# Kernel optimization log

Measured on AMD Instinct MI355X. Metric: run time of the kernel, lower is better.

## Reference

```python
import jax, jax.numpy as jnp
import numpy as np
from jax import lax

NC = 80
REG_MAX = 16
BINS = REG_MAX + 1
RADIUS = 2.5
TOPK = 10
L_BOX, L_CLS, L_DFL = 7.5, 1.0, 1.5


def focal_bce(x, t, alpha=0.25, gamma=2.0):
    # numerically stable BCE-with-logits: max(x,0) - x*t + log1p(exp(-|x|))
    p = jax.nn.sigmoid(x)
    ce = jnp.maximum(x, 0.0) - x * t + jnp.log1p(jnp.exp(-jnp.abs(x)))
    p_t = p * t + (1.0 - p) * (1.0 - t)
    a_t = alpha * t + (1.0 - alpha) * (1.0 - t)
    return ce * a_t * (1.0 - p_t) ** gamma


def _level_loss(reg, cls, boxes, labels, stride):
    B, _, H, W = reg.shape
    HW = H * W
    G = boxes.shape[1]
    gy, gx = jnp.meshgrid(jnp.arange(H, dtype=jnp.float32), jnp.arange(W, dtype=jnp.float32), indexing='ij')
    centers = jnp.stack([gx + 0.5, gy + 0.5], -1).reshape(HW, 2)  # [HW,2]
    gt = boxes / stride  # [B,G,4]
    gctr = (gt[..., :2] + gt[..., 2:]) * 0.5  # [B,G,2]
    cx = centers[None, :, None, 0]
    cy = centers[None, :, None, 1]
    dl = cx - gt[:, None, :, 0]
    dt = cy - gt[:, None, :, 1]
    dr = gt[:, None, :, 2] - cx
    db = gt[:, None, :, 3] - cy
    in_gt = (dl > 0) & (dt > 0) & (dr > 0) & (db > 0)
    in_ctr = ((cx >= gctr[:, None, :, 0] - RADIUS) & (cx <= gctr[:, None, :, 0] + RADIUS)
              & (cy >= gctr[:, None, :, 1] - RADIUS) & (cy <= gctr[:, None, :, 1] + RADIUS))
    mask = in_gt & in_ctr  # [B,HW,G]
    any_pos = jnp.any(mask, axis=(1, 2))  # [B]
    # fallback: topk closest anchor centers per GT (smallest distance along point dim)
    dist = jnp.sqrt(((centers[None, :, None, :] - gctr[:, None, :, :]) ** 2).sum(-1))  # [B,HW,G]
    k = min(TOPK, HW)
    _, idx = lax.top_k(-jnp.swapaxes(dist, 1, 2), k)  # [B,G,k]
    fb = jnp.zeros((B, HW, G), bool).at[jnp.arange(B)[:, None, None], idx, jnp.arange(G)[None, :, None]].set(True)
    mask = jnp.where(any_pos[:, None, None], mask, fb)
    mf = mask.astype(jnp.float32)
    n_pos = mf.sum((1, 2))  # [B] (>=1 by construction of fallback)

    cls_flat = cls.transpose(0, 2, 3, 1).reshape(B, HW, NC)
    reg_flat = reg.transpose(0, 2, 3, 1).reshape(B, HW, 4, BINS)

    # ---- DFL ----
    ltrb = jnp.clip(jnp.stack([dl, dt, dr, db], -1), 0.0)  # [B,HW,G,4]
    tgt = jnp.clip(ltrb, 0.0, REG_MAX - 1e-4)
    lb = jnp.floor(tgt).astype(jnp.int32)
    rb = jnp.minimum(lb + 1, REG_MAX)
    wl = rb.astype(jnp.float32) - tgt
    wr = tgt - lb.astype(jnp.float32)
    logp = jax.nn.log_softmax(reg_flat, -1)  # [B,HW,4,BINS]
    bi = jnp.arange(B)[:, None, None, None]
    pi = jnp.arange(HW)[None, :, None, None]
    ki = jnp.arange(4)[None, None, None, :]
    dfl_pair = -(logp[bi, pi, ki, lb] * wl + logp[bi, pi, ki, rb] * wr)  # [B,HW,G,4]
    dfl = ((dfl_pair * mf[..., None]).sum((1, 2, 3)) / (n_pos * 4.0)).sum()

    # ---- box (IoU, detached as in original) ----
    prob = jax.nn.softmax(reg_flat, -1)
    d = (prob * jnp.arange(BINS, dtype=jnp.float32)).sum(-1)  # [B,HW,4]
    pcx = centers[None, :, 0]
    pcy = centers[None, :, 1]
    pred_box = jnp.stack([pcx - d[..., 0], pcy - d[..., 1], pcx + d[..., 2], pcy + d[..., 3]], -1)  # [B,HW,4]
    b1 = pred_box[:, :, None, :]
    b2 = gt[:, None, :, :]
    iw = jnp.clip(jnp.minimum(b1[..., 2:], b2[..., 2:]) - jnp.maximum(b1[..., :2], b2[..., :2]), 0.0)
    inter = iw[..., 0] * iw[..., 1]
    a1 = (b1[..., 2] - b1[..., 0]) * (b1[..., 3] - b1[..., 1])
    a2 = (b2[..., 2] - b2[..., 0]) * (b2[..., 3] - b2[..., 1])
    iou = lax.stop_gradient(inter / (a1 + a2 - inter + 1e-6))  # [B,HW,G]
    box = ((1.0 - iou) * mf).sum()

    # ---- cls (focal BCE, soft IoU targets). Decompose one-hot target:
    # per positive pair: sum_c f(logit_c,0) - f(logit_cls,0) + f(logit_cls,iou)
    fz = focal_bce(cls_flat, 0.0)  # [B,HW,NC]
    fz_sum = fz.sum(-1)  # [B,HW]
    bi2 = jnp.arange(B)[:, None, None]
    pi2 = jnp.arange(HW)[None, :, None]
    ci = labels[:, None, :]  # [B,1,G]
    cls_at = cls_flat[bi2, pi2, ci]  # [B,HW,G]
    fz_at = fz[bi2, pi2, ci]
    cls_pos = ((fz_sum[:, :, None] - fz_at + focal_bce(cls_at, iou)) * mf).sum()
    pos_pt = jnp.any(mask, -1)  # [B,HW]
    cls_neg = jnp.where(pos_pt, 0.0, fz_sum).sum()
    return box, cls_pos + cls_neg, dfl


def _total(reg0, cls0, reg1, cls1, reg2, cls2, gt_boxes, gt_labels):
    tb = tc = td = 0.0
    for r, c, s in ((reg0, cls0, 8.0), (reg1, cls1, 16.0), (reg2, cls2, 32.0)):
        b, cl, d = _level_loss(r, c, gt_boxes, gt_labels, s)
        tb = tb + b
        tc = tc + cl
        td = td + d
    loss = L_BOX * tb + L_CLS * tc + L_DFL * td
    return loss, tb, tc, td


def setup_inputs() -> dict:
    key = jax.random.key(0)
    ks = jax.random.split(key, 10)
    B, G = 16, 32
    d = {}
    for i, (h, w) in enumerate(((80, 80), (40, 40), (20, 20))):
        d[f'reg{i}'] = jax.random.normal(ks[2 * i], (B, 4 * BINS, h, w), jnp.float32)
        d[f'cls{i}'] = jax.random.normal(ks[2 * i + 1], (B, NC, h, w), jnp.float32)
    ctr = jax.random.uniform(ks[6], (B, G, 2), minval=0.0, maxval=640.0)
    wh = jax.random.uniform(ks[7], (B, G, 2), minval=16.0, maxval=160.0)
    x1y1 = jnp.clip(ctr - wh * 0.5, 0.0, 640.0)
    x2y2 = jnp.clip(ctr + wh * 0.5, 0.0, 640.0)
    d['gt_boxes'] = jnp.concatenate([x1y1, x2y2], -1)
    d['gt_labels'] = jax.random.randint(ks[8], (B, G), 0, NC, jnp.int32)
    return d


def reference(reg0, cls0, reg1, cls1, reg2, cls2, gt_boxes, gt_labels):
    return _total(reg0, cls0, reg1, cls1, reg2, cls2, gt_boxes, gt_labels)
```

## Files before the change

### kernel.cpp

```cpp
#include <hip/hip_runtime.h>
#include <math.h>

#define NCLS 80
#define BINS 17
#define REGMAX 16
#define NG 32
#define NB 16
#define KTOP 10
#define RAD 2.5f

#define WS_ACC   0
#define WS_NPOS  32
#define WS_DFLN  224
#define WS_ANYP  416
#define WS_CNT   608
#define WS_FB    640
#define NBLOCKS  (67 * 16)

__device__ __forceinline__ float focal0(float x) {
    float e   = __expf(-fabsf(x));
    float inv = 1.0f / (1.0f + e);
    float p   = (x >= 0.0f) ? inv : e * inv;
    float ce  = fmaxf(x, 0.0f) + __logf(1.0f + e);
    return ce * 0.75f * p * p;
}

__device__ __forceinline__ float focal_t(float x, float t) {
    float e   = __expf(-fabsf(x));
    float inv = 1.0f / (1.0f + e);
    float p   = (x >= 0.0f) ? inv : e * inv;
    float ce  = fmaxf(x, 0.0f) - x * t + __logf(1.0f + e);
    float pt  = p * t + (1.0f - p) * (1.0f - t);
    float at  = 0.25f * t + 0.75f * (1.0f - t);
    float om  = 1.0f - pt;
    return ce * at * om * om;
}

__global__ void k_prep(const float* __restrict__ gtb,
                       float* __restrict__ acc, float* __restrict__ npos,
                       float* __restrict__ dfln, int* __restrict__ anyp,
                       int* __restrict__ cnt, int* __restrict__ fb) {
    int lvl = blockIdx.x;
    int tid = threadIdx.x;
    int b = tid >> 5, g = tid & 31;
    int W = (lvl == 0) ? 80 : (lvl == 1 ? 40 : 20);
    float inv_s = (lvl == 0) ? 0.125f : (lvl == 1 ? 0.0625f : 0.03125f);
    if (lvl == 0) {
        if (tid < 2)  acc[tid] = 0.0f;
        if (tid < 48) { npos[tid] = 0.0f; dfln[tid] = 0.0f; }
        if (tid == 48) *cnt = 0;
    }
    __shared__ int s_any[NB];
    if (tid < NB) s_any[tid] = 0;
    __syncthreads();

    const float* bb = gtb + (b * NG + g) * 4;
    float x1 = bb[0] * inv_s, y1 = bb[1] * inv_s;
    float x2 = bb[2] * inv_s, y2 = bb[3] * inv_s;
    float gcx = (x1 + x2) * 0.5f, gcy = (y1 + y2) * 0.5f;
    int j0 = max((int)floorf(gcx) - 4, 0), j1 = min((int)floorf(gcx) + 4, W - 1);
    int i0 = max((int)floorf(gcy) - 4, 0), i1 = min((int)floorf(gcy) + 4, W - 1);
    bool any = false;
    for (int i = i0; i <= i1; ++i) {
        float cy = (float)i + 0.5f;
        for (int j = j0; j <= j1; ++j) {
            float cx = (float)j + 0.5f;
            bool m = (cx - x1 > 0.0f) && (cy - y1 > 0.0f) &&
                     (x2 - cx > 0.0f) && (y2 - cy > 0.0f) &&
                     (cx >= gcx - RAD) && (cx <= gcx + RAD) &&
                     (cy >= gcy - RAD) && (cy <= gcy + RAD);
            any = any || m;
        }
    }
    if (any) atomicOr(&s_any[b], 1);
    __syncthreads();
    if (g == 0) anyp[lvl * NB + b] = s_any[b];

    if (!s_any[b]) {
        float bd[KTOP]; int bi[KTOP];
        for (int t = 0; t < KTOP; ++t) { bd[t] = 3.0e38f; bi[t] = 0; }
        int HW = W * W;
        for (int p = 0; p < HW; ++p) {
            float cx = (float)(p % W) + 0.5f;
            float cy = (float)(p / W) + 0.5f;
            float dx = cx - gcx, dy = cy - gcy;
            float d = dx * dx + dy * dy;
            if (d < bd[KTOP - 1]) {
                int t = KTOP - 1;
                while (t > 0 && d < bd[t - 1]) { bd[t] = bd[t-1]; bi[t] = bi[t-1]; --t; }
                bd[t] = d; bi[t] = p;
            }
        }
        int* o = fb + ((lvl * NB + b) * NG + g) * KTOP;
        for (int t = 0; t < KTOP; ++t) o[t] = bi[t];
    }
}

__global__ __launch_bounds__(256, 4) void k_main_f(
    const float* __restrict__ reg0, const float* __restrict__ cls0,
    const float* __restrict__ reg1, const float* __restrict__ cls1,
    const float* __restrict__ reg2, const float* __restrict__ cls2,
    const float* __restrict__ gtb,  const int* __restrict__ lab,
    const int* __restrict__ anyp,   const int* __restrict__ fb,
    float* __restrict__ acc, float* __restrict__ npos, float* __restrict__ dfln,
    int* __restrict__ cnt, float* __restrict__ out)
{
    int bx = blockIdx.x;
    int b  = blockIdx.y;
    int lvl, tix, W; const float *regp, *clsp; float inv_s;
    if (bx < 50)      { lvl = 0; tix = bx;      W = 80; regp = reg0; clsp = cls0; inv_s = 0.125f;   }
    else if (bx < 63) { lvl = 1; tix = bx - 50; W = 40; regp = reg1; clsp = cls1; inv_s = 0.0625f;  }
    else              { lvl = 2; tix = bx - 63; W = 20; regp = reg2; clsp = cls2; inv_s = 0.03125f; }
    int HW = W * W;
    int tile = tix * 128;

    int lane = threadIdx.x & 63;
    int s    = threadIdx.x >> 6;
    int q0   = tile + 2 * lane;
    bool v   = q0 < HW;
    int qc   = v ? q0 : 0;
    int ri0  = qc / W, ci0 = qc - ri0 * W;
    float cx0 = (float)ci0 + 0.5f, cy0 = (float)ri0 + 0.5f;
    int ci1 = ci0 + 1, ri1 = ri0; if (ci1 == W) { ci1 = 0; ri1 = ri0 + 1; }
    float cx1 = (float)ci1 + 0.5f, cy1 = (float)ri1 + 0.5f;

    int base_r = (b * 4 * BINS) * HW + qc;
    int base_c = (b * NCLS) * HW + qc;

    __shared__ float s_dv[4][128], s_lz[4][128], s_fz[4][128];
    __shared__ unsigned char s_ps[4][128];
    __shared__ float s_bx[NG][6];
    __shared__ int   s_lab[NG];

    if (threadIdx.x < NG) {
        int g = threadIdx.x;
        float4 bb4 = *(const float4*)(gtb + (b * NG + g) * 4);
        float x1 = bb4.x * inv_s, y1 = bb4.y * inv_s;
        float x2 = bb4.z * inv_s, y2 = bb4.w * inv_s;
        s_bx[g][0] = x1; s_bx[g][1] = y1; s_bx[g][2] = x2; s_bx[g][3] = y2;
        s_bx[g][4] = (x1 + x2) * 0.5f; s_bx[g][5] = (y1 + y2) * 0.5f;
        s_lab[g] = lab[b * NG + g];
    }

    float2 rv[BINS];
#pragma unroll
    for (int t = 0; t < BINS; ++t)
        rv[t] = *(const float2*)(regp + base_r + (s * BINS + t) * HW);
    float2 cv[20];
#pragma unroll
    for (int t = 0; t < 20; ++t)
        cv[t] = *(const float2*)(clsp + base_c + (s * 20 + t) * HW);

    {
        float m0 = rv[0].x, m1 = rv[0].y;
#pragma unroll
        for (int t = 1; t < BINS; ++t) { m0 = fmaxf(m0, rv[t].x); m1 = fmaxf(m1, rv[t].y); }
        float sa = 0.f, ea = 0.f, sb = 0.f, eb = 0.f;
#pragma unroll
        for (int t = 0; t < BINS; ++t) {
            float a = __expf(rv[t].x - m0), c = __expf(rv[t].y - m1);
            sa += a; ea += a * (float)t; sb += c; eb += c * (float)t;
        }
        s_dv[s][2*lane]   = ea / sa;  s_lz[s][2*lane]   = __logf(sa) + m0;
        s_dv[s][2*lane+1] = eb / sb;  s_lz[s][2*lane+1] = __logf(sb) + m1;
    }
    {
        float fz0 = 0.f, fz1 = 0.f;
#pragma unroll
        for (int t = 0; t < 20; ++t) { fz0 += focal0(cv[t].x); fz1 += focal0(cv[t].y); }
        s_fz[s][2*lane] = fz0; s_fz[s][2*lane+1] = fz1;
    }
    __syncthreads();

    float dv0[4], lz0v[4], dv1[4], lz1v[4];
#pragma unroll
    for (int k = 0; k < 4; ++k) {
        dv0[k] = s_dv[k][2*lane];   lz0v[k] = s_lz[k][2*lane];
        dv1[k] = s_dv[k][2*lane+1]; lz1v[k] = s_lz[k][2*lane+1];
    }
    float fzs0 = s_fz[0][2*lane]   + s_fz[1][2*lane]   + s_fz[2][2*lane]   + s_fz[3][2*lane];
    float fzs1 = s_fz[0][2*lane+1] + s_fz[1][2*lane+1] + s_fz[2][2*lane+1] + s_fz[3][2*lane+1];

    float px1_0 = cx0 - dv0[0], py1_0 = cy0 - dv0[1];
    float px2_0 = cx0 + dv0[2], py2_0 = cy0 + dv0[3];
    float pa0 = (px2_0 - px1_0) * (py2_0 - py1_0);
    float px1_1 = cx1 - dv1[0], py1_1 = cy1 - dv1[1];
    float px2_1 = cx1 + dv1[2], py2_1 = cy1 + dv1[3];
    float pa1 = (px2_1 - px1_1) * (py2_1 - py1_1);

    bool anyb = anyp[lvl * NB + b] != 0;
    float bxa = 0.f, cla = 0.f, dfa = 0.f, np = 0.f;
    bool posi0 = false, posi1 = false;

#define HEAVY(G, CX, CY, DL, DT, DR, DB, PX1, PY1, PX2, PY2, PA, LZ, FZS, OFF) do { \
    float ix1 = fmaxf(PX1, x1), iy1 = fmaxf(PY1, y1);                    \
    float ix2 = fminf(PX2, x2), iy2 = fminf(PY2, y2);                    \
    float iw = fmaxf(ix2 - ix1, 0.f), ih = fmaxf(iy2 - iy1, 0.f);        \
    float inter = iw * ih;                                               \
    float ga = (x2 - x1) * (y2 - y1);                                    \
    float iou = inter / (PA + ga - inter + 1e-6f);                       \
    bxa += 1.f - iou; np += 1.f;                                         \
    float ltrb[4] = { DL, DT, DR, DB };                                  \
    _Pragma("unroll")                                                    \
    for (int k = 0; k < 4; ++k) {                                        \
        float tt = fminf(fmaxf(ltrb[k], 0.f), 15.9999f);                 \
        float lf = floorf(tt); int lb = (int)lf;                         \
        int rb = lb + 1 > REGMAX ? REGMAX : lb + 1;                      \
        float wl = (float)rb - tt, wr = tt - lf;                         \
        float xl = regp[base_r + OFF + (k * BINS + lb) * HW];            \
        float xr = regp[base_r + OFF + (k * BINS + rb) * HW];            \
        dfa -= (xl - LZ[k]) * wl + (xr - LZ[k]) * wr;                    \
    }                                                                    \
    int c = s_lab[G];                                                    \
    float xat = clsp[base_c + OFF + c * HW];                             \
    cla += FZS - focal0(xat) + focal_t(xat, iou);                        \
} while (0)

#define PROC_G(G, GEOM) do {                                             \
    float x1 = s_bx[G][0], y1 = s_bx[G][1];                              \
    float x2 = s_bx[G][2], y2 = s_bx[G][3];                              \
    float dl0 = cx0 - x1, dt0 = cy0 - y1, dr0 = x2 - cx0, db0 = y2 - cy0;\
    float dl1 = cx1 - x1, dt1 = cy1 - y1, dr1 = x2 - cx1, db1 = y2 - cy1;\
    bool m0, m1;                                                         \
    if (GEOM) {                                                          \
        float gx = s_bx[G][4], gy = s_bx[G][5];                          \
        m0 = (dl0 > 0.f) && (dt0 > 0.f) && (dr0 > 0.f) && (db0 > 0.f) && \
             (cx0 >= gx - RAD) && (cx0 <= gx + RAD) &&                   \
             (cy0 >= gy - RAD) && (cy0 <= gy + RAD);                     \
        m1 = (dl1 > 0.f) && (dt1 > 0.f) && (dr1 > 0.f) && (db1 > 0.f) && \
             (cx1 >= gx - RAD) && (cx1 <= gx + RAD) &&                   \
             (cy1 >= gy - RAD) && (cy1 <= gy + RAD);                     \
    } else {                                                             \
        const int* fbp = fb + ((lvl * NB + b) * NG + (G)) * KTOP;        \
        m0 = false; m1 = false;                                          \
        _Pragma("unroll")                                                \
        for (int t = 0; t < KTOP; ++t) {                                 \
            int f = fbp[t]; m0 = m0 || (f == q0); m1 = m1 || (f == q0+1);\
        }                                                                \
    }                                                                    \
    m0 = m0 && v; m1 = m1 && v;                                          \
    if (__any(m0 || m1)) {                                               \
        if (m0) HEAVY((G), cx0, cy0, dl0, dt0, dr0, db0,                 \
                      px1_0, py1_0, px2_0, py2_0, pa0, lz0v, fzs0, 0);   \
        if (m1) HEAVY((G), cx1, cy1, dl1, dt1, dr1, db1,                 \
                      px1_1, py1_1, px2_1, py2_1, pa1, lz1v, fzs1, 1);   \
    }                                                                    \
    posi0 = posi0 || m0; posi1 = posi1 || m1;                            \
} while (0)

    if (anyb) {
        int gg = lane & 31;
        float gy1 = s_bx[gg][1], gy2 = s_bx[gg][3], gcy = s_bx[gg][5];
        int r0 = tile / W;
        int r1 = min(tile + 127, HW - 1) / W;
        float cyLo = (float)r0 + 0.5f, cyHi = (float)r1 + 0.5f;
        bool act = (cyHi > gy1) && (gy2 > cyLo) &&
                   (cyHi >= gcy - RAD) && (cyLo <= gcy + RAD);
        unsigned long long bm = __ballot(act);
        unsigned m32 = (unsigned)(bm | (bm >> 32));
        int ord = 0;
        while (m32) {
            int g = __builtin_ctz(m32); m32 &= m32 - 1;
            if ((ord++ & 3) == s) PROC_G(g, true);
        }
    } else {
        for (int t = 0; t < 8; ++t) { int g = s * 8 + t; PROC_G(g, false); }
    }

    s_ps[s][2*lane] = posi0; s_ps[s][2*lane+1] = posi1;
    __syncthreads();
    if (s == 0) {
        int pg0 = s_ps[0][2*lane] | s_ps[1][2*lane] | s_ps[2][2*lane] | s_ps[3][2*lane];
        int pg1 = s_ps[0][2*lane+1] | s_ps[1][2*lane+1] | s_ps[2][2*lane+1] | s_ps[3][2*lane+1];
        if (v && !pg0) cla += fzs0;
        if (v && !pg1) cla += fzs1;
    }

    float v0 = bxa, v1 = cla, v2 = dfa, v3 = np;
    for (int off = 32; off > 0; off >>= 1) {
        v0 += __shfl_down(v0, off);
        v1 += __shfl_down(v1, off);
        v2 += __shfl_down(v2, off);
        v3 += __shfl_down(v3, off);
    }
    __shared__ float red[4][4];
    if (lane == 0) { red[s][0] = v0; red[s][1] = v1; red[s][2] = v2; red[s][3] = v3; }
    __syncthreads();
    if (threadIdx.x == 0) {
        float t0 = 0, t1 = 0, t2 = 0, t3 = 0;
        for (int w = 0; w < 4; ++w) {
            t0 += red[w][0]; t1 += red[w][1]; t2 += red[w][2]; t3 += red[w][3];
        }
        atomicAdd(&acc[0], t0);
        atomicAdd(&acc[1], t1);
        atomicAdd(&dfln[lvl * NB + b], t2);
        atomicAdd(&npos[lvl * NB + b], t3);
    }

    __shared__ int s_tick;
    if (threadIdx.x == 0) {
        __threadfence();
        s_tick = atomicAdd(cnt, 1);
    }
    __syncthreads();
    if (s_tick == NBLOCKS - 1 && threadIdx.x < 64) {
        float vs = 0.f;
        if (lane < 48) {
            float n = atomicAdd(&npos[lane], 0.0f);
            float d = atomicAdd(&dfln[lane], 0.0f);
            if (n > 0.f) vs = d / (n * 4.0f);
        }
        for (int off = 32; off > 0; off >>= 1) vs += __shfl_down(vs, off);
        if (lane == 0) {
            float tbv = atomicAdd(&acc[0], 0.0f);
            float tcv = atomicAdd(&acc[1], 0.0f);
            out[0] = 7.5f * tbv + tcv + 1.5f * vs;
            out[1] = tbv; out[2] = tcv; out[3] = vs;
        }
    }
}

extern "C" void kernel_launch(void* const* d_in, const int* in_sizes, int n_in,
                              void* d_out, int out_size, void* d_ws, size_t ws_size,
                              hipStream_t stream) {
    const float* reg0 = (const float*)d_in[0];
    const float* cls0 = (const float*)d_in[1];
    const float* reg1 = (const float*)d_in[2];
    const float* cls1 = (const float*)d_in[3];
    const float* reg2 = (const float*)d_in[4];
    const float* cls2 = (const float*)d_in[5];
    const float* gtb  = (const float*)d_in[6];
    const int*   lab  = (const int*)d_in[7];
    float* out = (float*)d_out;

    char*  ws   = (char*)d_ws;
    float* acc  = (float*)(ws + WS_ACC);
    float* npos = (float*)(ws + WS_NPOS);
    float* dfln = (float*)(ws + WS_DFLN);
    int*   anyp = (int*)(ws + WS_ANYP);
    int*   cnt  = (int*)(ws + WS_CNT);
    int*   fb   = (int*)(ws + WS_FB);

    k_prep<<<3, 512, 0, stream>>>(gtb, acc, npos, dfln, anyp, cnt, fb);
    k_main_f<<<dim3(67, NB), 256, 0, stream>>>(reg0, cls0, reg1, cls1, reg2, cls2,
                                               gtb, lab, anyp, fb,
                                               acc, npos, dfln, cnt, out);
}
```

Measured before the change: 69.30 us.

## Stage reg/cls tiles into LDS via direct global-to-LDS loads, halve tile size

Replaces per-thread float2 register loads with global_load_lds DMA of all 148 channel rows for a 64-pixel tile into shared memory, one pixel per lane. Positive-anchor DFL and class gathers now read from LDS instead of scattered global memory. The tile shrinks from 128 to 64 pixels, which doubles the grid to 132x16 blocks, and the occupancy hint is dropped from launch bounds. In exchange each block uses about 38KB of LDS, which may limit blocks per CU, and each global load is 4 bytes per lane instead of 8.

```diff
diff --git a/kernel.cpp b/kernel.cpp
--- a/kernel.cpp
+++ b/kernel.cpp
@@ -8,6 +8,9 @@
 #define NB 16
 #define KTOP 10
 #define RAD 2.5f
+#define NROWS 148
+#define RPW 37
+#define TILE 64
 
 #define WS_ACC   0
 #define WS_NPOS  32
@@ -15,7 +18,13 @@
 #define WS_ANYP  416
 #define WS_CNT   608
 #define WS_FB    640
-#define NBLOCKS  (67 * 16)
+#define NBLOCKS  (132 * 16)
+
+__device__ __forceinline__ void dma4(const float* g, float* l) {
+    __builtin_amdgcn_global_load_lds(
+        (__attribute__((address_space(1))) void*)(g),
+        (__attribute__((address_space(3))) void*)(l), 4, 0, 0);
+}
 
 __device__ __forceinline__ float focal0(float x) {
     float e   = __expf(-fabsf(x));
@@ -96,7 +105,7 @@
     }
 }
 
-__global__ __launch_bounds__(256, 4) void k_main_f(
+__global__ __launch_bounds__(256) void k_main_f(
     const float* __restrict__ reg0, const float* __restrict__ cls0,
     const float* __restrict__ reg1, const float* __restrict__ cls1,
     const float* __restrict__ reg2, const float* __restrict__ cls2,
@@ -108,27 +117,23 @@
     int bx = blockIdx.x;
     int b  = blockIdx.y;
     int lvl, tix, W; const float *regp, *clsp; float inv_s;
-    if (bx < 50)      { lvl = 0; tix = bx;      W = 80; regp = reg0; clsp = cls0; inv_s = 0.125f;   }
-    else if (bx < 63) { lvl = 1; tix = bx - 50; W = 40; regp = reg1; clsp = cls1; inv_s = 0.0625f;  }
-    else              { lvl = 2; tix = bx - 63; W = 20; regp = reg2; clsp = cls2; inv_s = 0.03125f; }
+    if (bx < 100)      { lvl = 0; tix = bx;       W = 80; regp = reg0; clsp = cls0; inv_s = 0.125f;   }
+    else if (bx < 125) { lvl = 1; tix = bx - 100; W = 40; regp = reg1; clsp = cls1; inv_s = 0.0625f;  }
+    else               { lvl = 2; tix = bx - 125; W = 20; regp = reg2; clsp = cls2; inv_s = 0.03125f; }
     int HW = W * W;
-    int tile = tix * 128;
+    int tile = tix * TILE;
 
     int lane = threadIdx.x & 63;
     int s    = threadIdx.x >> 6;
-    int q0   = tile + 2 * lane;
-    bool v   = q0 < HW;
-    int qc   = v ? q0 : 0;
-    int ri0  = qc / W, ci0 = qc - ri0 * W;
-    float cx0 = (float)ci0 + 0.5f, cy0 = (float)ri0 + 0.5f;
-    int ci1 = ci0 + 1, ri1 = ri0; if (ci1 == W) { ci1 = 0; ri1 = ri0 + 1; }
-    float cx1 = (float)ci1 + 0.5f, cy1 = (float)ri1 + 0.5f;
-
-    int base_r = (b * 4 * BINS) * HW + qc;
-    int base_c = (b * NCLS) * HW + qc;
-
-    __shared__ float s_dv[4][128], s_lz[4][128], s_fz[4][128];
-    __shared__ unsigned char s_ps[4][128];
+    int p    = tile + lane;
+    bool v   = p < HW;
+    int pc   = v ? p : 0;
+    int ri = pc / W, ci = pc - ri * W;
+    float cx = (float)ci + 0.5f, cy = (float)ri + 0.5f;
+
+    __shared__ float s_stage[NROWS * 64];
+    __shared__ float s_dv[4][64], s_lz[4][64], s_fz[4][64];
+    __shared__ unsigned char s_ps[4][64];
     __shared__ float s_bx[NG][6];
     __shared__ int   s_lab[NG];
 
@@ -142,117 +147,107 @@
         s_lab[g] = lab[b * NG + g];
     }
 
-    float2 rv[BINS];
-#pragma unroll
-    for (int t = 0; t < BINS; ++t)
-        rv[t] = *(const float2*)(regp + base_r + (s * BINS + t) * HW);
-    float2 cv[20];
-#pragma unroll
-    for (int t = 0; t < 20; ++t)
-        cv[t] = *(const float2*)(clsp + base_c + (s * 20 + t) * HW);
+    int pcl = min(tile + lane, HW - 1);
+#pragma unroll
+    for (int t = 0; t < RPW; ++t) {
+        int row = s * RPW + t;
+        const float* src = (row < 68) ? regp + (b * 68 + row) * HW + pcl
+                                      : clsp + (b * 80 + (row - 68)) * HW + pcl;
+        dma4(src, s_stage + row * 64);
+    }
+    asm volatile("s_waitcnt vmcnt(0)" ::: "memory");
+    __syncthreads();
+
+    const float* st = s_stage;
 
     {
-        float m0 = rv[0].x, m1 = rv[0].y;
-#pragma unroll
-        for (int t = 1; t < BINS; ++t) { m0 = fmaxf(m0, rv[t].x); m1 = fmaxf(m1, rv[t].y); }
-        float sa = 0.f, ea = 0.f, sb = 0.f, eb = 0.f;
+        float xv[BINS];
+#pragma unroll
+        for (int t = 0; t < BINS; ++t) xv[t] = st[(s * BINS + t) * 64 + lane];
+        float m = xv[0];
+#pragma unroll
+        for (int t = 1; t < BINS; ++t) m = fmaxf(m, xv[t]);
+        float sum = 0.f, ex = 0.f;
 #pragma unroll
         for (int t = 0; t < BINS; ++t) {
-            float a = __expf(rv[t].x - m0), c = __expf(rv[t].y - m1);
-            sa += a; ea += a * (float)t; sb += c; eb += c * (float)t;
-        }
-        s_dv[s][2*lane]   = ea / sa;  s_lz[s][2*lane]   = __logf(sa) + m0;
-        s_dv[s][2*lane+1] = eb / sb;  s_lz[s][2*lane+1] = __logf(sb) + m1;
+            float ee = __expf(xv[t] - m);
+            sum += ee; ex += ee * (float)t;
+        }
+        s_dv[s][lane] = ex / sum;
+        s_lz[s][lane] = __logf(sum) + m;
     }
     {
-        float fz0 = 0.f, fz1 = 0.f;
-#pragma unroll
-        for (int t = 0; t < 20; ++t) { fz0 += focal0(cv[t].x); fz1 += focal0(cv[t].y); }
-        s_fz[s][2*lane] = fz0; s_fz[s][2*lane+1] = fz1;
-    }
-    __syncthreads();
-
-    float dv0[4], lz0v[4], dv1[4], lz1v[4];
-#pragma unroll
-    for (int k = 0; k < 4; ++k) {
-        dv0[k] = s_dv[k][2*lane];   lz0v[k] = s_lz[k][2*lane];
-        dv1[k] = s_dv[k][2*lane+1]; lz1v[k] = s_lz[k][2*lane+1];
-    }
-    float fzs0 = s_fz[0][2*lane]   + s_fz[1][2*lane]   + s_fz[2][2*lane]   + s_fz[3][2*lane];
-    float fzs1 = s_fz[0][2*lane+1] + s_fz[1][2*lane+1] + s_fz[2][2*lane+1] + s_fz[3][2*lane+1];
-
-    float px1_0 = cx0 - dv0[0], py1_0 = cy0 - dv0[1];
-    float px2_0 = cx0 + dv0[2], py2_0 = cy0 + dv0[3];
-    float pa0 = (px2_0 - px1_0) * (py2_0 - py1_0);
-    float px1_1 = cx1 - dv1[0], py1_1 = cy1 - dv1[1];
-    float px2_1 = cx1 + dv1[2], py2_1 = cy1 + dv1[3];
-    float pa1 = (px2_1 - px1_1) * (py2_1 - py1_1);
+        float fz = 0.f;
+#pragma unroll
+        for (int t = 0; t < 20; ++t)
+            fz += focal0(st[(68 + s * 20 + t) * 64 + lane]);
+        s_fz[s][lane] = fz;
+    }
+    __syncthreads();
+
+    float dv[4], lz[4];
+#pragma unroll
+    for (int k = 0; k < 4; ++k) { dv[k] = s_dv[k][lane]; lz[k] = s_lz[k][lane]; }
+    float fzs = s_fz[0][lane] + s_fz[1][lane] + s_fz[2][lane] + s_fz[3][lane];
+
+    float px1 = cx - dv[0], py1 = cy - dv[1];
+    float px2 = cx + dv[2], py2 = cy + dv[3];
+    float pa = (px2 - px1) * (py2 - py1);
 
     bool anyb = anyp[lvl * NB + b] != 0;
     float bxa = 0.f, cla = 0.f, dfa = 0.f, np = 0.f;
-    bool posi0 = false, posi1 = false;
-
-#define HEAVY(G, CX, CY, DL, DT, DR, DB, PX1, PY1, PX2, PY2, PA, LZ, FZS, OFF) do { \
-    float ix1 = fmaxf(PX1, x1), iy1 = fmaxf(PY1, y1);                    \
-    float ix2 = fminf(PX2, x2), iy2 = fminf(PY2, y2);                    \
-    float iw = fmaxf(ix2 - ix1, 0.f), ih = fmaxf(iy2 - iy1, 0.f);        \
-    float inter = iw * ih;                                               \
-    float ga = (x2 - x1) * (y2 - y1);                                    \
-    float iou = inter / (PA + ga - inter + 1e-6f);                       \
-    bxa += 1.f - iou; np += 1.f;                                         \
-    float ltrb[4] = { DL, DT, DR, DB };                                  \
-    _Pragma("unroll")                                                    \
-    for (int k = 0; k < 4; ++k) {                                        \
-        float tt = fminf(fmaxf(ltrb[k], 0.f), 15.9999f);                 \
-        float lf = floorf(tt); int lb = (int)lf;                         \
-        int rb = lb + 1 > REGMAX ? REGMAX : lb + 1;                      \
-        float wl = (float)rb - tt, wr = tt - lf;                         \
-        float xl = regp[base_r + OFF + (k * BINS + lb) * HW];            \
-        float xr = regp[base_r + OFF + (k * BINS + rb) * HW];            \
-        dfa -= (xl - LZ[k]) * wl + (xr - LZ[k]) * wr;                    \
-    }                                                                    \
-    int c = s_lab[G];                                                    \
-    float xat = clsp[base_c + OFF + c * HW];                             \
-    cla += FZS - focal0(xat) + focal_t(xat, iou);                        \
-} while (0)
+    bool posi = false;
 
 #define PROC_G(G, GEOM) do {                                             \
     float x1 = s_bx[G][0], y1 = s_bx[G][1];                              \
     float x2 = s_bx[G][2], y2 = s_bx[G][3];                              \
-    float dl0 = cx0 - x1, dt0 = cy0 - y1, dr0 = x2 - cx0, db0 = y2 - cy0;\
-    float dl1 = cx1 - x1, dt1 = cy1 - y1, dr1 = x2 - cx1, db1 = y2 - cy1;\
-    bool m0, m1;                                                         \
+    float dl = cx - x1, dt = cy - y1, dr = x2 - cx, db = y2 - cy;        \
+    bool m;                                                              \
     if (GEOM) {                                                          \
         float gx = s_bx[G][4], gy = s_bx[G][5];                          \
-        m0 = (dl0 > 0.f) && (dt0 > 0.f) && (dr0 > 0.f) && (db0 > 0.f) && \
-             (cx0 >= gx - RAD) && (cx0 <= gx + RAD) &&                   \
-             (cy0 >= gy - RAD) && (cy0 <= gy + RAD);                     \
-        m1 = (dl1 > 0.f) && (dt1 > 0.f) && (dr1 > 0.f) && (db1 > 0.f) && \
-             (cx1 >= gx - RAD) && (cx1 <= gx + RAD) &&                   \
-             (cy1 >= gy - RAD) && (cy1 <= gy + RAD);                     \
+        m = (dl > 0.f) && (dt > 0.f) && (dr > 0.f) && (db > 0.f) &&      \
+            (cx >= gx - RAD) && (cx <= gx + RAD) &&                      \
+            (cy >= gy - RAD) && (cy <= gy + RAD);                        \
     } else {                                                             \
         const int* fbp = fb + ((lvl * NB + b) * NG + (G)) * KTOP;        \
-        m0 = false; m1 = false;                                          \
+        m = false;                                                       \
         _Pragma("unroll")                                                \
-        for (int t = 0; t < KTOP; ++t) {                                 \
-            int f = fbp[t]; m0 = m0 || (f == q0); m1 = m1 || (f == q0+1);\
+        for (int t = 0; t < KTOP; ++t) m = m || (fbp[t] == p);           \
+    }                                                                    \
+    m = m && v;                                                          \
+    if (__any(m)) {                                                      \
+        if (m) {                                                         \
+            float ix1 = fmaxf(px1, x1), iy1 = fmaxf(py1, y1);            \
+            float ix2 = fminf(px2, x2), iy2 = fminf(py2, y2);            \
+            float iw = fmaxf(ix2 - ix1, 0.f), ih = fmaxf(iy2 - iy1, 0.f);\
+            float inter = iw * ih;                                       \
+            float ga = (x2 - x1) * (y2 - y1);                            \
+            float iou = inter / (pa + ga - inter + 1e-6f);               \
+            bxa += 1.f - iou; np += 1.f;                                 \
+            float ltrb[4] = { dl, dt, dr, db };                          \
+            _Pragma("unroll")                                            \
+            for (int k = 0; k < 4; ++k) {                                \
+                float tt = fminf(fmaxf(ltrb[k], 0.f), 15.9999f);         \
+                float lf = floorf(tt); int lb = (int)lf;                 \
+                int rb = lb + 1 > REGMAX ? REGMAX : lb + 1;              \
+                float wl = (float)rb - tt, wr = tt - lf;                 \
+                float xl = st[(k * BINS + lb) * 64 + lane];              \
+                float xr = st[(k * BINS + rb) * 64 + lane];              \
+                dfa -= (xl - lz[k]) * wl + (xr - lz[k]) * wr;            \
+            }                                                            \
+            int c = s_lab[G];                                            \
+            float xat = st[(68 + c) * 64 + lane];                        \
+            cla += fzs - focal0(xat) + focal_t(xat, iou);                \
         }                                                                \
     }                                                                    \
-    m0 = m0 && v; m1 = m1 && v;                                          \
-    if (__any(m0 || m1)) {                                               \
-        if (m0) HEAVY((G), cx0, cy0, dl0, dt0, dr0, db0,                 \
-                      px1_0, py1_0, px2_0, py2_0, pa0, lz0v, fzs0, 0);   \
-        if (m1) HEAVY((G), cx1, cy1, dl1, dt1, dr1, db1,                 \
-                      px1_1, py1_1, px2_1, py2_1, pa1, lz1v, fzs1, 1);   \
-    }                                                                    \
-    posi0 = posi0 || m0; posi1 = posi1 || m1;                            \
+    posi = posi || m;                                                    \
 } while (0)
 
     if (anyb) {
         int gg = lane & 31;
         float gy1 = s_bx[gg][1], gy2 = s_bx[gg][3], gcy = s_bx[gg][5];
         int r0 = tile / W;
-        int r1 = min(tile + 127, HW - 1) / W;
+        int r1 = min(tile + TILE - 1, HW - 1) / W;
         float cyLo = (float)r0 + 0.5f, cyHi = (float)r1 + 0.5f;
         bool act = (cyHi > gy1) && (gy2 > cyLo) &&
                    (cyHi >= gcy - RAD) && (cyLo <= gcy + RAD);
@@ -267,13 +262,11 @@
         for (int t = 0; t < 8; ++t) { int g = s * 8 + t; PROC_G(g, false); }
     }
 
-    s_ps[s][2*lane] = posi0; s_ps[s][2*lane+1] = posi1;
+    s_ps[s][lane] = posi;
     __syncthreads();
     if (s == 0) {
-        int pg0 = s_ps[0][2*lane] | s_ps[1][2*lane] | s_ps[2][2*lane] | s_ps[3][2*lane];
-        int pg1 = s_ps[0][2*lane+1] | s_ps[1][2*lane+1] | s_ps[2][2*lane+1] | s_ps[3][2*lane+1];
-        if (v && !pg0) cla += fzs0;
-        if (v && !pg1) cla += fzs1;
+        int pg = s_ps[0][lane] | s_ps[1][lane] | s_ps[2][lane] | s_ps[3][lane];
+        if (v && !pg) cla += fzs;
     }
 
     float v0 = bxa, v1 = cla, v2 = dfa, v3 = np;
@@ -342,7 +335,7 @@
     int*   fb   = (int*)(ws + WS_FB);
 
     k_prep<<<3, 512, 0, stream>>>(gtb, acc, npos, dfln, anyp, cnt, fb);
-    k_main_f<<<dim3(67, NB), 256, 0, stream>>>(reg0, cls0, reg1, cls1, reg2, cls2,
-                                               gtb, lab, anyp, fb,
-                                               acc, npos, dfln, cnt, out);
-}
+    k_main_f<<<dim3(132, NB), 256, 0, stream>>>(reg0, cls0, reg1, cls1, reg2, cls2,
+                                                gtb, lab, anyp, fb,
+                                                acc, npos, dfln, cnt, out);
+}
```

Result: slower. 99.55 us (+43.6%).

## Split block into 8 waves separating DFL softmax and focal-sum work

Applied to the files above, without the earlier changes.

Doubles the block to 512 threads: waves 0-3 load and reduce regression bins while waves 4-7 stream class logits and compute the zero-target focal sum. Per-GT matching work is spread over 8 waves instead of 4. The aim is to cut per-thread register footprint (no longer holding 37 float2 values) and raise latency hiding. The cost is larger blocks, more shared-memory reductions and heavier per-wave matching under launch bounds of 512x8.

```diff
diff --git a/kernel.cpp b/kernel.cpp
--- a/kernel.cpp
+++ b/kernel.cpp
@@ -96,7 +96,7 @@
     }
 }
 
-__global__ __launch_bounds__(256, 4) void k_main_f(
+__global__ __launch_bounds__(512, 8) void k_main_f(
     const float* __restrict__ reg0, const float* __restrict__ cls0,
     const float* __restrict__ reg1, const float* __restrict__ cls1,
     const float* __restrict__ reg2, const float* __restrict__ cls2,
@@ -118,17 +118,17 @@
     int s    = threadIdx.x >> 6;
     int q0   = tile + 2 * lane;
     bool v   = q0 < HW;
-    int qc   = v ? q0 : 0;
-    int ri0  = qc / W, ci0 = qc - ri0 * W;
+    int pc   = v ? q0 : 0;
+    int ri0  = pc / W, ci0 = pc - ri0 * W;
     float cx0 = (float)ci0 + 0.5f, cy0 = (float)ri0 + 0.5f;
     int ci1 = ci0 + 1, ri1 = ri0; if (ci1 == W) { ci1 = 0; ri1 = ri0 + 1; }
     float cx1 = (float)ci1 + 0.5f, cy1 = (float)ri1 + 0.5f;
 
-    int base_r = (b * 4 * BINS) * HW + qc;
-    int base_c = (b * NCLS) * HW + qc;
+    int base_r = (b * 4 * BINS) * HW + pc;
+    int base_c = (b * NCLS) * HW + pc;
 
     __shared__ float s_dv[4][128], s_lz[4][128], s_fz[4][128];
-    __shared__ unsigned char s_ps[4][128];
+    __shared__ unsigned char s_ps[8][128];
     __shared__ float s_bx[NG][6];
     __shared__ int   s_lab[NG];
 
@@ -142,33 +142,31 @@
         s_lab[g] = lab[b * NG + g];
     }
 
-    float2 rv[BINS];
-#pragma unroll
-    for (int t = 0; t < BINS; ++t)
-        rv[t] = *(const float2*)(regp + base_r + (s * BINS + t) * HW);
-    float2 cv[20];
-#pragma unroll
-    for (int t = 0; t < 20; ++t)
-        cv[t] = *(const float2*)(clsp + base_c + (s * 20 + t) * HW);
-
-    {
+    if (s < 4) {
+        float2 rv[BINS];
+#pragma unroll
+        for (int t = 0; t < BINS; ++t)
+            rv[t] = *(const float2*)(regp + base_r + (s * BINS + t) * HW);
         float m0 = rv[0].x, m1 = rv[0].y;
 #pragma unroll
         for (int t = 1; t < BINS; ++t) { m0 = fmaxf(m0, rv[t].x); m1 = fmaxf(m1, rv[t].y); }
         float sa = 0.f, ea = 0.f, sb = 0.f, eb = 0.f;
 #pragma unroll
         for (int t = 0; t < BINS; ++t) {
-            float a = __expf(rv[t].x - m0), c = __expf(rv[t].y - m1);
-            sa += a; ea += a * (float)t; sb += c; eb += c * (float)t;
+            float a = __expf(rv[t].x - m0), cc = __expf(rv[t].y - m1);
+            sa += a; ea += a * (float)t; sb += cc; eb += cc * (float)t;
         }
         s_dv[s][2*lane]   = ea / sa;  s_lz[s][2*lane]   = __logf(sa) + m0;
         s_dv[s][2*lane+1] = eb / sb;  s_lz[s][2*lane+1] = __logf(sb) + m1;
-    }
-    {
+    } else {
+        int coff = (s - 4) * 20;
         float fz0 = 0.f, fz1 = 0.f;
 #pragma unroll
-        for (int t = 0; t < 20; ++t) { fz0 += focal0(cv[t].x); fz1 += focal0(cv[t].y); }
-        s_fz[s][2*lane] = fz0; s_fz[s][2*lane+1] = fz1;
+        for (int t = 0; t < 20; ++t) {
+            float2 c2 = *(const float2*)(clsp + base_c + (coff + t) * HW);
+            fz0 += focal0(c2.x); fz1 += focal0(c2.y);
+        }
+        s_fz[s - 4][2*lane] = fz0; s_fz[s - 4][2*lane+1] = fz1;
     }
     __syncthreads();
 
@@ -211,8 +209,8 @@
         float xr = regp[base_r + OFF + (k * BINS + rb) * HW];            \
         dfa -= (xl - LZ[k]) * wl + (xr - LZ[k]) * wr;                    \
     }                                                                    \
-    int c = s_lab[G];                                                    \
-    float xat = clsp[base_c + OFF + c * HW];                             \
+    int cc2 = s_lab[G];                                                  \
+    float xat = clsp[base_c + OFF + cc2 * HW];                           \
     cla += FZS - focal0(xat) + focal_t(xat, iou);                        \
 } while (0)
 
@@ -261,17 +259,19 @@
         int ord = 0;
         while (m32) {
             int g = __builtin_ctz(m32); m32 &= m32 - 1;
-            if ((ord++ & 3) == s) PROC_G(g, true);
+            if ((ord++ & 7) == s) PROC_G(g, true);
         }
     } else {
-        for (int t = 0; t < 8; ++t) { int g = s * 8 + t; PROC_G(g, false); }
+#pragma unroll
+        for (int t = 0; t < 4; ++t) { int g = s * 4 + t; PROC_G(g, false); }
     }
 
     s_ps[s][2*lane] = posi0; s_ps[s][2*lane+1] = posi1;
     __syncthreads();
     if (s == 0) {
-        int pg0 = s_ps[0][2*lane] | s_ps[1][2*lane] | s_ps[2][2*lane] | s_ps[3][2*lane];
-        int pg1 = s_ps[0][2*lane+1] | s_ps[1][2*lane+1] | s_ps[2][2*lane+1] | s_ps[3][2*lane+1];
+        int pg0 = 0, pg1 = 0;
+#pragma unroll
+        for (int w = 0; w < 8; ++w) { pg0 |= s_ps[w][2*lane]; pg1 |= s_ps[w][2*lane+1]; }
         if (v && !pg0) cla += fzs0;
         if (v && !pg1) cla += fzs1;
     }
@@ -283,12 +283,12 @@
         v2 += __shfl_down(v2, off);
         v3 += __shfl_down(v3, off);
     }
-    __shared__ float red[4][4];
+    __shared__ float red[8][4];
     if (lane == 0) { red[s][0] = v0; red[s][1] = v1; red[s][2] = v2; red[s][3] = v3; }
     __syncthreads();
     if (threadIdx.x == 0) {
         float t0 = 0, t1 = 0, t2 = 0, t3 = 0;
-        for (int w = 0; w < 4; ++w) {
+        for (int w = 0; w < 8; ++w) {
             t0 += red[w][0]; t1 += red[w][1]; t2 += red[w][2]; t3 += red[w][3];
         }
         atomicAdd(&acc[0], t0);
@@ -342,7 +342,7 @@
     int*   fb   = (int*)(ws + WS_FB);
 
     k_prep<<<3, 512, 0, stream>>>(gtb, acc, npos, dfln, anyp, cnt, fb);
-    k_main_f<<<dim3(67, NB), 256, 0, stream>>>(reg0, cls0, reg1, cls1, reg2, cls2,
+    k_main_f<<<dim3(67, NB), 512, 0, stream>>>(reg0, cls0, reg1, cls1, reg2, cls2,
                                                gtb, lab, anyp, fb,
                                                acc, npos, dfln, cnt, out);
 }
```

New measurement: 72.42 us. 4.5% more time.
